# Kernel tuning notes

Measured on AMD Instinct MI355X. Metric: run time of the kernel, lower is better.

The kernel has to match this reference:

```python
import jax, jax.numpy as jnp
import numpy as np
import math

NEG_INF = -1e29
B, L, H = 16, 1024, 512
D = 2 * H          # feature dim of s and q
GELU_C = math.sqrt(2.0 / math.pi)


def gelu(x):
    return 0.5 * x * (1.0 + jnp.tanh(GELU_C * (x + 0.044715 * x ** 3)))


def mask_softmax(W, m1, m2):
    # joint mask: [B, len1, 1] * [B, 1, len2]
    m = (m1[:, :, None] * m2[:, None, :]).astype(W.dtype)
    return jax.nn.softmax(W + (1.0 - m) * NEG_INF, axis=-1)


def heuristic(x, y, w_r, b_r, w_g, b_g):
    inp = jnp.concatenate([x, y, x * y, x - y], axis=-1)  # [B, L, 8H]
    r = gelu(inp @ w_r.T + b_r)                           # [B, L, 2H]
    g = jax.nn.sigmoid(inp @ w_g.T + b_g)
    return g * r + (1.0 - g) * x


def setup_inputs() -> dict:
    key = jax.random.key(0)
    k = jax.random.split(key, 6)
    s = jax.random.normal(k[0], (B, L, D), jnp.float32)
    q = jax.random.normal(k[1], (B, L, D), jnp.float32)
    s_mask = jnp.ones((B, L), jnp.int32)
    q_mask = jnp.ones((B, L), jnp.int32)
    fan_in = 8 * H
    lim = 1.0 / np.sqrt(fan_in)
    w_r = jax.random.uniform(k[2], (2 * H, fan_in), jnp.float32, -lim, lim)
    b_r = jax.random.uniform(k[3], (2 * H,), jnp.float32, -lim, lim)
    w_g = jax.random.uniform(k[4], (2 * H, fan_in), jnp.float32, -lim, lim)
    b_g = jax.random.uniform(k[5], (2 * H,), jnp.float32, -lim, lim)
    return {"s": s, "q": q, "w_r": w_r, "b_r": b_r, "w_g": w_g, "b_g": b_g,
            "s_mask": s_mask, "q_mask": q_mask}


def reference(s, q, w_r, b_r, w_g, b_g, s_mask, q_mask):
    a = jnp.einsum('bsd,btd->bst', s, q)                  # [B, Ls, Lq]
    b = mask_softmax(a, s_mask, q_mask) @ q               # [B, Ls, D]
    c = mask_softmax(a.swapaxes(-1, -2), q_mask, s_mask) @ s  # [B, Lq, D]
    s_tilde = heuristic(s, b, w_r, b_r, w_g, b_g)
    q_tilde = heuristic(q, c, w_r, b_r, w_g, b_g)
    return (s_tilde, q_tilde)
```

## Files before the change

kernel.cpp:

```cpp
#include <hip/hip_runtime.h>
#include <hip/hip_bf16.h>
#include <math.h>

#define DEVI static __device__ __forceinline__

typedef unsigned short u16;
typedef unsigned int u32;
typedef __bf16 bf16_t;
typedef bf16_t bf16x8 __attribute__((ext_vector_type(8)));
typedef float f32x4 __attribute__((ext_vector_type(4)));

static constexpr int Bb = 16;
static constexpr int L  = 1024;
static constexpr int D  = 1024;
static constexpr int KH = 4096;

DEVI u16 f2bf(float f) {
  union { float f; u32 u; } v; v.f = f;
  u32 r = v.u + 0x7FFFu + ((v.u >> 16) & 1u);
  return (u16)(r >> 16);
}

DEVI float bf2f(u16 b) {
  union { u32 u; float f; } v; v.u = ((u32)b) << 16;
  return v.f;
}

DEVI void gload16(const void* g, void* l) {
  __builtin_amdgcn_global_load_lds((const __attribute__((address_space(1))) u32*)g,
                                   (__attribute__((address_space(3))) u32*)l,
                                   16, 0, 0);
}

DEVI int swz(int row, int col) { return col ^ ((row & 7) << 3); }

__global__ void k_cast_bf16(const float* __restrict__ in, u16* __restrict__ out, int n4) {
  int i = blockIdx.x * blockDim.x + threadIdx.x;
  int stride = gridDim.x * blockDim.x;
  for (; i < n4; i += stride) {
    float4 v = ((const float4*)in)[i];
    ushort4 o;
    o.x = f2bf(v.x); o.y = f2bf(v.y); o.z = f2bf(v.z); o.w = f2bf(v.w);
    ((ushort4*)out)[i] = o;
  }
}

__global__ void k_cast_split(const float* __restrict__ in, u16* __restrict__ hi,
                             u16* __restrict__ lo, int n4) {
  int i = blockIdx.x * blockDim.x + threadIdx.x;
  int stride = gridDim.x * blockDim.x;
  for (; i < n4; i += stride) {
    float4 v = ((const float4*)in)[i];
    ushort4 h, l;
    h.x = f2bf(v.x); h.y = f2bf(v.y); h.z = f2bf(v.z); h.w = f2bf(v.w);
    l.x = f2bf(v.x - bf2f(h.x));
    l.y = f2bf(v.y - bf2f(h.y));
    l.z = f2bf(v.z - bf2f(h.z));
    l.w = f2bf(v.w - bf2f(h.w));
    ((ushort4*)hi)[i] = h;
    ((ushort4*)lo)[i] = l;
  }
}

__global__ __launch_bounds__(256)
void k_transpose_bf16(const float* __restrict__ in, u16* __restrict__ out) {
  __shared__ float tile[32][33];
  int b = blockIdx.z;
  int d0 = blockIdx.x * 32;
  int l0 = blockIdx.y * 32;
  const float* ip = in + (size_t)b * L * D;
  u16* op = out + (size_t)b * L * D;
  int tx = threadIdx.x, ty = threadIdx.y;
  #pragma unroll
  for (int j = 0; j < 4; ++j)
    tile[ty + 8 * j][tx] = ip[(size_t)(l0 + ty + 8 * j) * D + d0 + tx];
  __syncthreads();
  #pragma unroll
  for (int j = 0; j < 4; ++j)
    op[(size_t)(d0 + ty + 8 * j) * L + l0 + tx] = f2bf(tile[tx][ty + 8 * j]);
}

template<int OUT_BF16>
__global__ __launch_bounds__(256, 4)
void k_gemm_nt(const u16* __restrict__ A, const u16* __restrict__ Bm, void* __restrict__ Cv,
               int K, int ldc, size_t sA, size_t sB, size_t sC, int tilesN)
{
  __shared__ __align__(16) u16 As[128 * 64];
  __shared__ __align__(16) u16 Bs[128 * 64];
  const int bx = blockIdx.x;
  const int tm = bx / tilesN, tn = bx % tilesN;
  const int b = blockIdx.y;
  const u16* Ap = A + (size_t)b * sA + (size_t)tm * 128 * K;
  const u16* Bp = Bm + (size_t)b * sB + (size_t)tn * 128 * K;
  const int tid = threadIdx.x;
  const int lane = tid & 63, wv = tid >> 6;
  const int wm = wv >> 1, wn = wv & 1;
  const int srow = tid >> 3;
  const int scol = (tid & 7) * 8;
  const int scolswz = swz(srow, scol);
  f32x4 acc[4][4] = {};
  for (int k0 = 0; k0 < K; k0 += 64) {
    #pragma unroll
    for (int i = 0; i < 4; ++i) {
      int row = i * 32 + srow;
      gload16(Ap + (size_t)row * K + k0 + scolswz, &As[row * 64 + scol]);
    }
    #pragma unroll
    for (int i = 0; i < 4; ++i) {
      int row = i * 32 + srow;
      gload16(Bp + (size_t)row * K + k0 + scolswz, &Bs[row * 64 + scol]);
    }
    __syncthreads();
    const int hi8 = (lane >> 4) * 8;
    #pragma unroll
    for (int kk = 0; kk < 64; kk += 32) {
      bf16x8 af[4], bfv[4];
      #pragma unroll
      for (int m = 0; m < 4; ++m) {
        int rr = wm * 64 + m * 16 + (lane & 15);
        af[m] = *(const bf16x8*)&As[rr * 64 + swz(rr, kk + hi8)];
      }
      #pragma unroll
      for (int n = 0; n < 4; ++n) {
        int rr = wn * 64 + n * 16 + (lane & 15);
        bfv[n] = *(const bf16x8*)&Bs[rr * 64 + swz(rr, kk + hi8)];
      }
      #pragma unroll
      for (int m = 0; m < 4; ++m)
        #pragma unroll
        for (int n = 0; n < 4; ++n)
          acc[m][n] = __builtin_amdgcn_mfma_f32_16x16x32_bf16(af[m], bfv[n], acc[m][n], 0, 0, 0);
    }
    __syncthreads();
  }
  const int rb = tm * 128 + wm * 64 + ((lane >> 4) << 2);
  const int cb = tn * 128 + wn * 64 + (lane & 15);
  #pragma unroll
  for (int m = 0; m < 4; ++m)
    #pragma unroll
    for (int n = 0; n < 4; ++n)
      #pragma unroll
      for (int j = 0; j < 4; ++j) {
        int r = rb + m * 16 + j, c = cb + n * 16;
        if (OUT_BF16)
          ((u16*)Cv)[(size_t)b * sC + (size_t)r * ldc + c] = f2bf(acc[m][n][j]);
        else
          ((float*)Cv)[(size_t)b * sC + (size_t)r * ldc + c] = acc[m][n][j];
      }
}

__global__ __launch_bounds__(256, 2)
void k_gemm_nt_split(const u16* __restrict__ Ah, const u16* __restrict__ Al,
                     const u16* __restrict__ Bh, const u16* __restrict__ Bl,
                     float* __restrict__ C, int K, int ldc, size_t sAB, size_t sC, int tilesN)
{
  __shared__ __align__(16) u16 Ahs[128 * 64];
  __shared__ __align__(16) u16 Als[128 * 64];
  __shared__ __align__(16) u16 Bhs[128 * 64];
  __shared__ __align__(16) u16 Bls[128 * 64];
  const int bx = blockIdx.x;
  const int tm = bx / tilesN, tn = bx % tilesN;
  const int b = blockIdx.y;
  const size_t aoff = (size_t)b * sAB + (size_t)tm * 128 * K;
  const size_t boff = (size_t)b * sAB + (size_t)tn * 128 * K;
  const int tid = threadIdx.x;
  const int lane = tid & 63, wv = tid >> 6;
  const int wm = wv >> 1, wn = wv & 1;
  const int srow = tid >> 3;
  const int scol = (tid & 7) * 8;
  const int scolswz = swz(srow, scol);
  f32x4 acc[4][4] = {};
  for (int k0 = 0; k0 < K; k0 += 64) {
    #pragma unroll
    for (int i = 0; i < 4; ++i) {
      int row = i * 32 + srow;
      size_t ga = aoff + (size_t)row * K + k0 + scolswz;
      size_t gb = boff + (size_t)row * K + k0 + scolswz;
      int ls = row * 64 + scol;
      gload16(Ah + ga, &Ahs[ls]);
      gload16(Al + ga, &Als[ls]);
      gload16(Bh + gb, &Bhs[ls]);
      gload16(Bl + gb, &Bls[ls]);
    }
    __syncthreads();
    const int hi8 = (lane >> 4) * 8;
    #pragma unroll
    for (int kk = 0; kk < 64; kk += 32) {
      bf16x8 ah[4], al[4], bh[4], bl[4];
      #pragma unroll
      for (int m = 0; m < 4; ++m) {
        int rr = wm * 64 + m * 16 + (lane & 15);
        int off = rr * 64 + swz(rr, kk + hi8);
        ah[m] = *(const bf16x8*)&Ahs[off];
        al[m] = *(const bf16x8*)&Als[off];
      }
      #pragma unroll
      for (int n = 0; n < 4; ++n) {
        int rr = wn * 64 + n * 16 + (lane & 15);
        int off = rr * 64 + swz(rr, kk + hi8);
        bh[n] = *(const bf16x8*)&Bhs[off];
        bl[n] = *(const bf16x8*)&Bls[off];
      }
      #pragma unroll
      for (int m = 0; m < 4; ++m)
        #pragma unroll
        for (int n = 0; n < 4; ++n) {
          acc[m][n] = __builtin_amdgcn_mfma_f32_16x16x32_bf16(ah[m], bh[n], acc[m][n], 0, 0, 0);
          acc[m][n] = __builtin_amdgcn_mfma_f32_16x16x32_bf16(ah[m], bl[n], acc[m][n], 0, 0, 0);
          acc[m][n] = __builtin_amdgcn_mfma_f32_16x16x32_bf16(al[m], bh[n], acc[m][n], 0, 0, 0);
        }
    }
    __syncthreads();
  }
  const int rb = tm * 128 + wm * 64 + ((lane >> 4) << 2);
  const int cb = tn * 128 + wn * 64 + (lane & 15);
  #pragma unroll
  for (int m = 0; m < 4; ++m)
    #pragma unroll
    for (int n = 0; n < 4; ++n)
      #pragma unroll
      for (int j = 0; j < 4; ++j) {
        int r = rb + m * 16 + j, c = cb + n * 16;
        C[(size_t)b * sC + (size_t)r * ldc + c] = acc[m][n][j];
      }
}

__global__ __launch_bounds__(256)
void k_row_softmax(const float* __restrict__ a, u16* __restrict__ P,
                   const int* __restrict__ m1, const int* __restrict__ m2)
{
  const int row = blockIdx.x, b = blockIdx.y;
  const float* ar = a + ((size_t)b * L + row) * L;
  const int tid = threadIdx.x, lane = tid & 63, wv = tid >> 6;
  __shared__ float redm[4], reds[4];
  float4 v = ((const float4*)ar)[tid];
  int4 mv = ((const int4*)(m2 + (size_t)b * L))[tid];
  const int mr = m1[(size_t)b * L + row];
  float x0 = v.x + (float)(1 - mr * mv.x) * (-1e29f);
  float x1 = v.y + (float)(1 - mr * mv.y) * (-1e29f);
  float x2 = v.z + (float)(1 - mr * mv.z) * (-1e29f);
  float x3 = v.w + (float)(1 - mr * mv.w) * (-1e29f);
  float mx = fmaxf(fmaxf(x0, x1), fmaxf(x2, x3));
  #pragma unroll
  for (int o = 32; o > 0; o >>= 1) mx = fmaxf(mx, __shfl_xor(mx, o));
  if (lane == 0) redm[wv] = mx;
  __syncthreads();
  mx = fmaxf(fmaxf(redm[0], redm[1]), fmaxf(redm[2], redm[3]));
  float e0 = __expf(x0 - mx), e1 = __expf(x1 - mx), e2 = __expf(x2 - mx), e3 = __expf(x3 - mx);
  float s4 = e0 + e1 + e2 + e3;
  #pragma unroll
  for (int o = 32; o > 0; o >>= 1) s4 += __shfl_xor(s4, o);
  if (lane == 0) reds[wv] = s4;
  __syncthreads();
  float inv = 1.0f / (reds[0] + reds[1] + reds[2] + reds[3]);
  ushort4 o;
  o.x = f2bf(e0 * inv); o.y = f2bf(e1 * inv); o.z = f2bf(e2 * inv); o.w = f2bf(e3 * inv);
  ((ushort4*)(P + ((size_t)b * L + row) * L))[tid] = o;
}

__global__ __launch_bounds__(256)
void k_col_softmax(const float* __restrict__ a, u16* __restrict__ P,
                   const int* __restrict__ mrow, const int* __restrict__ mcol)
{
  __shared__ float mred[4][64], lred[4][64];
  __shared__ float Mc[64], Li[64];
  __shared__ u16 T[64][68];
  const int b = blockIdx.y;
  const int c0 = blockIdx.x * 64;
  const int tid = threadIdx.x;
  const int cl = tid & 63;
  const int qr = tid >> 6;
  const int c = c0 + cl;
  const float* ab = a + (size_t)b * L * L;
  const int mc = mcol[(size_t)b * L + c];
  const int* msk = mrow + (size_t)b * L;
  float m = -3.0e38f, l = 0.0f;
  for (int r = qr * 256; r < qr * 256 + 256; ++r) {
    float x = ab[(size_t)r * L + c] + (float)(1 - mc * msk[r]) * (-1e29f);
    float mn = fmaxf(m, x);
    l = l * __expf(m - mn) + __expf(x - mn);
    m = mn;
  }
  mred[qr][cl] = m; lred[qr][cl] = l;
  __syncthreads();
  if (tid < 64) {
    float M = fmaxf(fmaxf(mred[0][tid], mred[1][tid]), fmaxf(mred[2][tid], mred[3][tid]));
    float Lt = lred[0][tid] * __expf(mred[0][tid] - M) + lred[1][tid] * __expf(mred[1][tid] - M)
             + lred[2][tid] * __expf(mred[2][tid] - M) + lred[3][tid] * __expf(mred[3][tid] - M);
    Mc[tid] = M; Li[tid] = 1.0f / Lt;
  }
  __syncthreads();
  const float M = Mc[cl], Linv = Li[cl];
  u16* Pb = P + (size_t)b * L * L;
  const int tl = tid >> 2, sc = (tid & 3) * 16;
  for (int ch = 0; ch < 16; ++ch) {
    #pragma unroll
    for (int rs = 0; rs < 16; ++rs) {
      int r = ch * 64 + qr * 16 + rs;
      float x = ab[(size_t)r * L + c] + (float)(1 - mc * msk[r]) * (-1e29f);
      T[cl][qr * 16 + rs] = f2bf(__expf(x - M) * Linv);
    }
    __syncthreads();
    ushort4* d4 = (ushort4*)(Pb + (size_t)(c0 + tl) * L + ch * 64 + sc);
    #pragma unroll
    for (int jj = 0; jj < 4; ++jj) {
      ushort4 v;
      v.x = T[tl][sc + jj * 4 + 0]; v.y = T[tl][sc + jj * 4 + 1];
      v.z = T[tl][sc + jj * 4 + 2]; v.w = T[tl][sc + jj * 4 + 3];
      d4[jj] = v;
    }
    __syncthreads();
  }
}

__global__ __launch_bounds__(512, 2)
void k_heur2(const u16* __restrict__ Xbf, const u16* __restrict__ Ybf,
             const u16* __restrict__ Wr, const u16* __restrict__ Wg,
             const float* __restrict__ br, const float* __restrict__ bg,
             const float* __restrict__ Xf, float* __restrict__ out)
{
  __shared__ __align__(16) u16 Xs[256 * 64];
  __shared__ __align__(16) u16 Ys[256 * 64];
  __shared__ __align__(16) u16 Ws[2][2][128 * 64];
  const int bx = blockIdx.x;
  const int xcd = bx & 7, li = bx >> 3;
  const int tn = li & 7, tm = xcd * 8 + (li >> 3);
  const size_t rowBase = (size_t)tm * 256;
  const int tid = threadIdx.x, lane = tid & 63;
  const int wv = tid >> 6;
  const int wm = wv >> 1, wn = wv & 1;
  const int srow = tid >> 3;
  const int scol = (tid & 7) * 8;
  const int scolswz = swz(srow, scol);
  f32x4 accR[4][4] = {}, accG[4][4] = {};

  for (int g = 0; g < 16; ++g) {
    const int c0 = g * 64;
    #pragma unroll
    for (int i = 0; i < 4; ++i) {
      int row = i * 64 + srow;
      size_t goff = (rowBase + row) * (size_t)D + c0 + scolswz;
      gload16(Xbf + goff, &Xs[row * 64 + scol]);
      gload16(Ybf + goff, &Ys[row * 64 + scol]);
    }
    #pragma unroll
    for (int i = 0; i < 2; ++i) {
      int row = i * 64 + srow;
      size_t woff = ((size_t)tn * 128 + row) * (size_t)KH + c0 + scolswz;
      gload16(Wr + woff, &Ws[0][0][row * 64 + scol]);
      gload16(Wg + woff, &Ws[0][1][row * 64 + scol]);
    }
    __syncthreads();
    #pragma unroll
    for (int ft = 0; ft < 4; ++ft) {
      const int cur = ft & 1;
      if (ft < 3) {
        #pragma unroll
        for (int i = 0; i < 2; ++i) {
          int row = i * 64 + srow;
          size_t woff = ((size_t)tn * 128 + row) * (size_t)KH + ((ft + 1) * 1024 + c0) + scolswz;
          gload16(Wr + woff, &Ws[cur ^ 1][0][row * 64 + scol]);
          gload16(Wg + woff, &Ws[cur ^ 1][1][row * 64 + scol]);
        }
      }
      const int hi8 = (lane >> 4) * 8;
      #pragma unroll
      for (int kk = 0; kk < 64; kk += 32) {
        bf16x8 af[4];
        #pragma unroll
        for (int m = 0; m < 4; ++m) {
          int rr = wm * 64 + m * 16 + (lane & 15);
          int off = rr * 64 + swz(rr, kk + hi8);
          if (ft == 0) af[m] = *(const bf16x8*)&Xs[off];
          else if (ft == 1) af[m] = *(const bf16x8*)&Ys[off];
          else {
            bf16x8 xv = *(const bf16x8*)&Xs[off];
            bf16x8 yv = *(const bf16x8*)&Ys[off];
            bf16x8 f;
            #pragma unroll
            for (int j = 0; j < 8; ++j) {
              float xf2 = (float)xv[j], yf2 = (float)yv[j];
              f[j] = (bf16_t)((ft == 2) ? xf2 * yf2 : xf2 - yf2);
            }
            af[m] = f;
          }
        }
        #pragma unroll
        for (int n = 0; n < 4; ++n) {
          int rr = wn * 64 + n * 16 + (lane & 15);
          int off = rr * 64 + swz(rr, kk + hi8);
          bf16x8 bR = *(const bf16x8*)&Ws[cur][0][off];
          bf16x8 bG = *(const bf16x8*)&Ws[cur][1][off];
          #pragma unroll
          for (int m = 0; m < 4; ++m) {
            accR[m][n] = __builtin_amdgcn_mfma_f32_16x16x32_bf16(af[m], bR, accR[m][n], 0, 0, 0);
            accG[m][n] = __builtin_amdgcn_mfma_f32_16x16x32_bf16(af[m], bG, accG[m][n], 0, 0, 0);
          }
        }
      }
      __syncthreads();
    }
  }
  const int rb = wm * 64 + ((lane >> 4) << 2);
  const int cb = tn * 128 + wn * 64 + (lane & 15);
  #pragma unroll
  for (int m = 0; m < 4; ++m)
    #pragma unroll
    for (int n = 0; n < 4; ++n)
      #pragma unroll
      for (int j = 0; j < 4; ++j) {
        size_t row = rowBase + rb + m * 16 + j;
        int col = cb + n * 16;
        float r = accR[m][n][j] + br[col];
        float g = accG[m][n][j] + bg[col];
        float t = tanhf(0.79788456080286535588f * (r + 0.044715f * r * r * r));
        float gl = 0.5f * r * (1.0f + t);
        float sg = 1.0f / (1.0f + __expf(-g));
        float xv = Xf[row * (size_t)D + col];
        out[row * (size_t)D + col] = sg * gl + (1.0f - sg) * xv;
      }
}

extern "C" void kernel_launch(void* const* d_in, const int* in_sizes, int n_in,
                              void* d_out, int out_size, void* d_ws, size_t ws_size,
                              hipStream_t stream)
{
  (void)in_sizes; (void)n_in; (void)out_size; (void)ws_size;
  const float* s    = (const float*)d_in[0];
  const float* q    = (const float*)d_in[1];
  const float* w_r  = (const float*)d_in[2];
  const float* b_r  = (const float*)d_in[3];
  const float* w_g  = (const float*)d_in[4];
  const float* b_g  = (const float*)d_in[5];
  const int* s_mask = (const int*)d_in[6];
  const int* q_mask = (const int*)d_in[7];
  float* out = (float*)d_out;

  const size_t SQ = (size_t)Bb * L * D;
  const size_t W  = (size_t)D * KH;
  const size_t S1 = (size_t)L * D;

  char* p = (char*)d_ws;
  u16* s_bf  = (u16*)p; p += SQ * 2;
  u16* q_bf  = (u16*)p; p += SQ * 2;
  u16* buf1  = (u16*)p; p += SQ * 2;
  u16* buf2  = (u16*)p; p += SQ * 2;
  u16* b_bf  = (u16*)p; p += SQ * 2;
  u16* c_bf  = (u16*)p; p += SQ * 2;
  u16* wr_bf = (u16*)p; p += W * 2;
  u16* wg_bf = (u16*)p; p += W * 2;

  float* a  = out;
  u16*   P1 = (u16*)(out + SQ);
  u16*   P2 = (u16*)(out + SQ + SQ / 2);

  dim3 blk(256);
  k_cast_split<<<4096, blk, 0, stream>>>(s, s_bf, buf1, (int)(SQ / 4));
  k_cast_split<<<4096, blk, 0, stream>>>(q, q_bf, buf2, (int)(SQ / 4));
  k_cast_bf16<<<2048, blk, 0, stream>>>(w_r, wr_bf, (int)(W / 4));
  k_cast_bf16<<<2048, blk, 0, stream>>>(w_g, wg_bf, (int)(W / 4));

  dim3 ggrid(64, Bb);
  k_gemm_nt_split<<<ggrid, blk, 0, stream>>>(s_bf, buf1, q_bf, buf2, a, D, L, S1, (size_t)L * L, 8);
  k_row_softmax<<<dim3(L, Bb), blk, 0, stream>>>(a, P1, s_mask, q_mask);
  k_col_softmax<<<dim3(L / 64, Bb), blk, 0, stream>>>(a, P2, s_mask, q_mask);

  dim3 tgrid(D / 32, L / 32, Bb), tblk(32, 8);
  k_transpose_bf16<<<tgrid, tblk, 0, stream>>>(s, buf1);
  k_transpose_bf16<<<tgrid, tblk, 0, stream>>>(q, buf2);

  k_gemm_nt<1><<<ggrid, blk, 0, stream>>>(P1, buf2, b_bf, L, D, (size_t)L * L, S1, S1, 8);
  k_gemm_nt<1><<<ggrid, blk, 0, stream>>>(P2, buf1, c_bf, L, D, (size_t)L * L, S1, S1, 8);

  k_heur2<<<512, dim3(512), 0, stream>>>(s_bf, b_bf, wr_bf, wg_bf, b_r, b_g, s, out);
  k_heur2<<<512, dim3(512), 0, stream>>>(q_bf, c_bf, wr_bf, wg_bf, b_r, b_g, q, out + SQ);
}
```

Measured before the change: 1.060 ms.

## Interleave gate and residual weights and precompute heuristic features for single-GEMM tile

Interleaves the rows of w_r and w_g into one bf16 weight matrix so each output tile computes the r and g columns together with a single accumulator set. A new elementwise kernel precomputes x*y and x-y into buffers, so the GEMM no longer builds those features in its inner loop. The GEMM is restructured to 256x256 tiles with K-step 32, double-buffered LDS, explicit waitcnt and barrier scheduling, and priority boosts around the MFMAs. The epilogue pairs r and g through a lane shuffle, and only even lanes store. In exchange it adds extra global writes and reads for the feature buffers, and half the lanes do redundant epilogue work.

```diff
diff --git a/kernel.cpp b/kernel.cpp
--- a/kernel.cpp
+++ b/kernel.cpp
@@ -59,6 +59,40 @@
     l.w = f2bf(v.w - bf2f(h.w));
     ((ushort4*)hi)[i] = h;
     ((ushort4*)lo)[i] = l;
+  }
+}
+
+__global__ void k_wcat(const float* __restrict__ wr, const float* __restrict__ wg,
+                       u16* __restrict__ wcat, int n4) {
+  int i = blockIdx.x * blockDim.x + threadIdx.x;
+  int stride = gridDim.x * blockDim.x;
+  for (; i < n4; i += stride) {
+    int j = i >> 10;
+    int c4 = i & 1023;
+    const float* src = ((j & 1) ? wg : wr) + (size_t)(j >> 1) * 4096 + c4 * 4;
+    float4 v = *(const float4*)src;
+    ushort4 o;
+    o.x = f2bf(v.x); o.y = f2bf(v.y); o.z = f2bf(v.z); o.w = f2bf(v.w);
+    ((ushort4*)wcat)[i] = o;
+  }
+}
+
+__global__ void k_feat(const u16* __restrict__ x, const u16* __restrict__ y,
+                       u16* __restrict__ xy, u16* __restrict__ xmy, int n8) {
+  int i = blockIdx.x * blockDim.x + threadIdx.x;
+  int stride = gridDim.x * blockDim.x;
+  for (; i < n8; i += stride) {
+    bf16x8 xv = ((const bf16x8*)x)[i];
+    bf16x8 yv = ((const bf16x8*)y)[i];
+    bf16x8 p, d;
+    #pragma unroll
+    for (int j = 0; j < 8; ++j) {
+      float xf = (float)xv[j], yf = (float)yv[j];
+      p[j] = (bf16_t)(xf * yf);
+      d[j] = (bf16_t)(xf - yf);
+    }
+    ((bf16x8*)xy)[i] = p;
+    ((bf16x8*)xmy)[i] = d;
   }
 }
 
@@ -314,111 +348,107 @@
 }
 
 __global__ __launch_bounds__(512, 2)
-void k_heur2(const u16* __restrict__ Xbf, const u16* __restrict__ Ybf,
-             const u16* __restrict__ Wr, const u16* __restrict__ Wg,
-             const float* __restrict__ br, const float* __restrict__ bg,
-             const float* __restrict__ Xf, float* __restrict__ out)
+void k_gemm_heur(const u16* __restrict__ X, const u16* __restrict__ Y,
+                 const u16* __restrict__ XY, const u16* __restrict__ XMY,
+                 const u16* __restrict__ Wc,
+                 const float* __restrict__ br, const float* __restrict__ bg,
+                 const float* __restrict__ Xf, float* __restrict__ out)
 {
-  __shared__ __align__(16) u16 Xs[256 * 64];
-  __shared__ __align__(16) u16 Ys[256 * 64];
-  __shared__ __align__(16) u16 Ws[2][2][128 * 64];
+  __shared__ __align__(16) u16 As[2][256 * 32];
+  __shared__ __align__(16) u16 Bs[2][256 * 32];
   const int bx = blockIdx.x;
   const int xcd = bx & 7, li = bx >> 3;
   const int tn = li & 7, tm = xcd * 8 + (li >> 3);
   const size_t rowBase = (size_t)tm * 256;
-  const int tid = threadIdx.x, lane = tid & 63;
-  const int wv = tid >> 6;
-  const int wm = wv >> 1, wn = wv & 1;
-  const int srow = tid >> 3;
-  const int scol = (tid & 7) * 8;
-  const int scolswz = swz(srow, scol);
-  f32x4 accR[4][4] = {}, accG[4][4] = {};
-
-  for (int g = 0; g < 16; ++g) {
-    const int c0 = g * 64;
-    #pragma unroll
-    for (int i = 0; i < 4; ++i) {
-      int row = i * 64 + srow;
-      size_t goff = (rowBase + row) * (size_t)D + c0 + scolswz;
-      gload16(Xbf + goff, &Xs[row * 64 + scol]);
-      gload16(Ybf + goff, &Ys[row * 64 + scol]);
-    }
-    #pragma unroll
-    for (int i = 0; i < 2; ++i) {
-      int row = i * 64 + srow;
-      size_t woff = ((size_t)tn * 128 + row) * (size_t)KH + c0 + scolswz;
-      gload16(Wr + woff, &Ws[0][0][row * 64 + scol]);
-      gload16(Wg + woff, &Ws[0][1][row * 64 + scol]);
-    }
-    __syncthreads();
-    #pragma unroll
-    for (int ft = 0; ft < 4; ++ft) {
-      const int cur = ft & 1;
-      if (ft < 3) {
-        #pragma unroll
-        for (int i = 0; i < 2; ++i) {
-          int row = i * 64 + srow;
-          size_t woff = ((size_t)tn * 128 + row) * (size_t)KH + ((ft + 1) * 1024 + c0) + scolswz;
-          gload16(Wr + woff, &Ws[cur ^ 1][0][row * 64 + scol]);
-          gload16(Wg + woff, &Ws[cur ^ 1][1][row * 64 + scol]);
-        }
-      }
-      const int hi8 = (lane >> 4) * 8;
-      #pragma unroll
-      for (int kk = 0; kk < 64; kk += 32) {
-        bf16x8 af[4];
-        #pragma unroll
-        for (int m = 0; m < 4; ++m) {
-          int rr = wm * 64 + m * 16 + (lane & 15);
-          int off = rr * 64 + swz(rr, kk + hi8);
-          if (ft == 0) af[m] = *(const bf16x8*)&Xs[off];
-          else if (ft == 1) af[m] = *(const bf16x8*)&Ys[off];
-          else {
-            bf16x8 xv = *(const bf16x8*)&Xs[off];
-            bf16x8 yv = *(const bf16x8*)&Ys[off];
-            bf16x8 f;
-            #pragma unroll
-            for (int j = 0; j < 8; ++j) {
-              float xf2 = (float)xv[j], yf2 = (float)yv[j];
-              f[j] = (bf16_t)((ft == 2) ? xf2 * yf2 : xf2 - yf2);
-            }
-            af[m] = f;
-          }
-        }
-        #pragma unroll
-        for (int n = 0; n < 4; ++n) {
-          int rr = wn * 64 + n * 16 + (lane & 15);
-          int off = rr * 64 + swz(rr, kk + hi8);
-          bf16x8 bR = *(const bf16x8*)&Ws[cur][0][off];
-          bf16x8 bG = *(const bf16x8*)&Ws[cur][1][off];
-          #pragma unroll
-          for (int m = 0; m < 4; ++m) {
-            accR[m][n] = __builtin_amdgcn_mfma_f32_16x16x32_bf16(af[m], bR, accR[m][n], 0, 0, 0);
-            accG[m][n] = __builtin_amdgcn_mfma_f32_16x16x32_bf16(af[m], bG, accG[m][n], 0, 0, 0);
-          }
-        }
-      }
-      __syncthreads();
-    }
-  }
-  const int rb = wm * 64 + ((lane >> 4) << 2);
-  const int cb = tn * 128 + wn * 64 + (lane & 15);
-  #pragma unroll
-  for (int m = 0; m < 4; ++m)
-    #pragma unroll
-    for (int n = 0; n < 4; ++n)
+  const int colBase = tn * 256;
+  const int tid = threadIdx.x, lane = tid & 63, wv = tid >> 6;
+  const int wm = wv >> 2, wn = wv & 3;
+
+  const int sidx0 = (wv * 2 + 0) * 64 + lane;
+  const int sidx1 = (wv * 2 + 1) * 64 + lane;
+  const int arow0 = sidx0 >> 2, arow1 = sidx1 >> 2;
+  const int asl0 = (sidx0 & 3) ^ ((arow0 >> 1) & 3);
+  const int asl1 = (sidx1 & 3) ^ ((arow1 >> 1) & 3);
+  const size_t aoff0 = (rowBase + arow0) * (size_t)D + asl0 * 8;
+  const size_t aoff1 = (rowBase + arow1) * (size_t)D + asl1 * 8;
+  const size_t boff0 = (size_t)(colBase + arow0) * KH + asl0 * 8;
+  const size_t boff1 = (size_t)(colBase + arow1) * KH + asl1 * 8;
+
+  f32x4 acc[8][4] = {};
+
+#define HSTAGE(T, BUF) do {                                                    \
+    int kk0 = (T) * 32;                                                        \
+    const u16* ap = (kk0 < 2048) ? (kk0 < 1024 ? X : Y)                        \
+                                 : (kk0 < 3072 ? XY : XMY);                    \
+    int kc = kk0 & 1023;                                                       \
+    gload16(ap + aoff0 + kc, &As[BUF][sidx0 * 8]);                             \
+    gload16(ap + aoff1 + kc, &As[BUF][sidx1 * 8]);                             \
+    gload16(Wc + boff0 + kk0, &Bs[BUF][sidx0 * 8]);                            \
+    gload16(Wc + boff1 + kk0, &Bs[BUF][sidx1 * 8]);                            \
+  } while (0)
+
+  HSTAGE(0, 0);
+  for (int t = 0; t < 128; ++t) {
+    const int cur = t & 1;
+    asm volatile("" ::: "memory");
+    __builtin_amdgcn_s_barrier();
+    asm volatile("" ::: "memory");
+    if (t + 1 < 128) {
+      HSTAGE(t + 1, cur ^ 1);
+      asm volatile("s_waitcnt vmcnt(4)" ::: "memory");
+    } else {
+      asm volatile("s_waitcnt vmcnt(0)" ::: "memory");
+    }
+    asm volatile("" ::: "memory");
+    __builtin_amdgcn_s_barrier();
+    asm volatile("" ::: "memory");
+
+    bf16x8 af[8], bfv[4];
+    #pragma unroll
+    for (int m = 0; m < 8; ++m) {
+      int rr = wm * 128 + m * 16 + (lane & 15);
+      int sp = (lane >> 4) ^ ((rr >> 1) & 3);
+      af[m] = *(const bf16x8*)&As[cur][rr * 32 + sp * 8];
+    }
+    #pragma unroll
+    for (int n = 0; n < 4; ++n) {
+      int rr = wn * 64 + n * 16 + (lane & 15);
+      int sp = (lane >> 4) ^ ((rr >> 1) & 3);
+      bfv[n] = *(const bf16x8*)&Bs[cur][rr * 32 + sp * 8];
+    }
+    __builtin_amdgcn_s_setprio(1);
+    #pragma unroll
+    for (int m = 0; m < 8; ++m)
+      #pragma unroll
+      for (int n = 0; n < 4; ++n)
+        acc[m][n] = __builtin_amdgcn_mfma_f32_16x16x32_bf16(af[m], bfv[n], acc[m][n], 0, 0, 0);
+    __builtin_amdgcn_s_setprio(0);
+  }
+#undef HSTAGE
+
+  const int odd = lane & 1;
+  #pragma unroll
+  for (int m = 0; m < 8; ++m)
+    #pragma unroll
+    for (int n = 0; n < 4; ++n) {
+      int ncol = colBase + wn * 64 + n * 16 + (lane & 15);
+      int c = ncol >> 1;
       #pragma unroll
       for (int j = 0; j < 4; ++j) {
-        size_t row = rowBase + rb + m * 16 + j;
-        int col = cb + n * 16;
-        float r = accR[m][n][j] + br[col];
-        float g = accG[m][n][j] + bg[col];
-        float t = tanhf(0.79788456080286535588f * (r + 0.044715f * r * r * r));
-        float gl = 0.5f * r * (1.0f + t);
+        size_t row = rowBase + wm * 128 + m * 16 + ((lane >> 4) << 2) + j;
+        float v = acc[m][n][j];
+        float pv = __shfl_xor(v, 1);
+        float r = odd ? pv : v;
+        float g = odd ? v : pv;
+        r += br[c]; g += bg[c];
+        float th = tanhf(0.79788456080286535588f * (r + 0.044715f * r * r * r));
+        float gl = 0.5f * r * (1.0f + th);
         float sg = 1.0f / (1.0f + __expf(-g));
-        float xv = Xf[row * (size_t)D + col];
-        out[row * (size_t)D + col] = sg * gl + (1.0f - sg) * xv;
-      }
+        float xv = Xf[row * (size_t)D + c];
+        float res = sg * gl + (1.0f - sg) * xv;
+        if (!odd) out[row * (size_t)D + c] = res;
+      }
+    }
 }
 
 extern "C" void kernel_launch(void* const* d_in, const int* in_sizes, int n_in,
@@ -447,8 +477,7 @@
   u16* buf2  = (u16*)p; p += SQ * 2;
   u16* b_bf  = (u16*)p; p += SQ * 2;
   u16* c_bf  = (u16*)p; p += SQ * 2;
-  u16* wr_bf = (u16*)p; p += W * 2;
-  u16* wg_bf = (u16*)p; p += W * 2;
+  u16* wcat  = (u16*)p; p += 2 * W * 2;
 
   float* a  = out;
   u16*   P1 = (u16*)(out + SQ);
@@ -457,8 +486,7 @@
   dim3 blk(256);
   k_cast_split<<<4096, blk, 0, stream>>>(s, s_bf, buf1, (int)(SQ / 4));
   k_cast_split<<<4096, blk, 0, stream>>>(q, q_bf, buf2, (int)(SQ / 4));
-  k_cast_bf16<<<2048, blk, 0, stream>>>(w_r, wr_bf, (int)(W / 4));
-  k_cast_bf16<<<2048, blk, 0, stream>>>(w_g, wg_bf, (int)(W / 4));
+  k_wcat<<<4096, blk, 0, stream>>>(w_r, w_g, wcat, (int)(2 * W / 4));
 
   dim3 ggrid(64, Bb);
   k_gemm_nt_split<<<ggrid, blk, 0, stream>>>(s_bf, buf1, q_bf, buf2, a, D, L, S1, (size_t)L * L, 8);
@@ -472,6 +500,9 @@
   k_gemm_nt<1><<<ggrid, blk, 0, stream>>>(P1, buf2, b_bf, L, D, (size_t)L * L, S1, S1, 8);
   k_gemm_nt<1><<<ggrid, blk, 0, stream>>>(P2, buf1, c_bf, L, D, (size_t)L * L, S1, S1, 8);
 
-  k_heur2<<<512, dim3(512), 0, stream>>>(s_bf, b_bf, wr_bf, wg_bf, b_r, b_g, s, out);
-  k_heur2<<<512, dim3(512), 0, stream>>>(q_bf, c_bf, wr_bf, wg_bf, b_r, b_g, q, out + SQ);
-}
+  k_feat<<<2048, blk, 0, stream>>>(s_bf, b_bf, buf1, buf2, (int)(SQ / 8));
+  k_gemm_heur<<<512, dim3(512), 0, stream>>>(s_bf, b_bf, buf1, buf2, wcat, b_r, b_g, s, out);
+
+  k_feat<<<2048, blk, 0, stream>>>(q_bf, c_bf, buf1, buf2, (int)(SQ / 8));
+  k_gemm_heur<<<512, dim3(512), 0, stream>>>(q_bf, c_bf, buf1, buf2, wcat, b_r, b_g, q, out + SQ);
+}
```

Measured after the change: 1.274 ms. 20.2% more time.

## Flatten heuristic GEMM K-loop into a software-pipelined schedule with explicit waitcnts

Applied to the files above, without the earlier changes.

Replaces the nested group/feature loop of the heuristic GEMM with one flat 64-step loop. Weight tiles are prefetched two steps ahead into the double buffer, and the next X/Y tile is loaded after the last feature step, using explicit vmcnt/lgkmcnt waits and raw s_barrier instead of __syncthreads. MFMA bursts are wrapped in s_setprio so compute waves win issue priority. The aim is to overlap global loads with MFMA work and cut barrier stalls; correctness now depends on the hand-counted wait values.

```diff
diff --git a/kernel.cpp b/kernel.cpp
--- a/kernel.cpp
+++ b/kernel.cpp
@@ -334,73 +334,113 @@
   const int scolswz = swz(srow, scol);
   f32x4 accR[4][4] = {}, accG[4][4] = {};
 
-  for (int g = 0; g < 16; ++g) {
-    const int c0 = g * 64;
-    #pragma unroll
-    for (int i = 0; i < 4; ++i) {
-      int row = i * 64 + srow;
-      size_t goff = (rowBase + row) * (size_t)D + c0 + scolswz;
-      gload16(Xbf + goff, &Xs[row * 64 + scol]);
-      gload16(Ybf + goff, &Ys[row * 64 + scol]);
-    }
+  #pragma unroll
+  for (int i = 0; i < 4; ++i) {
+    int row = i * 64 + srow;
+    size_t goff = (rowBase + row) * (size_t)D + scolswz;
+    gload16(Xbf + goff, &Xs[row * 64 + scol]);
+    gload16(Ybf + goff, &Ys[row * 64 + scol]);
+  }
+  #pragma unroll
+  for (int i = 0; i < 2; ++i) {
+    int row = i * 64 + srow;
+    size_t woff = ((size_t)tn * 128 + row) * (size_t)KH + scolswz;
+    gload16(Wr + woff, &Ws[0][0][row * 64 + scol]);
+    gload16(Wg + woff, &Ws[0][1][row * 64 + scol]);
+  }
+  asm volatile("s_waitcnt vmcnt(0)" ::: "memory");
+  __builtin_amdgcn_sched_barrier(0);
+  __builtin_amdgcn_s_barrier();
+  __builtin_amdgcn_sched_barrier(0);
+  {
     #pragma unroll
     for (int i = 0; i < 2; ++i) {
       int row = i * 64 + srow;
-      size_t woff = ((size_t)tn * 128 + row) * (size_t)KH + c0 + scolswz;
-      gload16(Wr + woff, &Ws[0][0][row * 64 + scol]);
-      gload16(Wg + woff, &Ws[0][1][row * 64 + scol]);
-    }
-    __syncthreads();
-    #pragma unroll
-    for (int ft = 0; ft < 4; ++ft) {
-      const int cur = ft & 1;
-      if (ft < 3) {
-        #pragma unroll
-        for (int i = 0; i < 2; ++i) {
-          int row = i * 64 + srow;
-          size_t woff = ((size_t)tn * 128 + row) * (size_t)KH + ((ft + 1) * 1024 + c0) + scolswz;
-          gload16(Wr + woff, &Ws[cur ^ 1][0][row * 64 + scol]);
-          gload16(Wg + woff, &Ws[cur ^ 1][1][row * 64 + scol]);
+      size_t woff = ((size_t)tn * 128 + row) * (size_t)KH + 1024 + scolswz;
+      gload16(Wr + woff, &Ws[1][0][row * 64 + scol]);
+      gload16(Wg + woff, &Ws[1][1][row * 64 + scol]);
+    }
+  }
+
+  for (int t = 0; t < 64; ++t) {
+    const int cur = t & 1;
+    const int ft = t & 3;
+
+    if (t > 0 && ft == 0) {
+      asm volatile("s_waitcnt vmcnt(4)" ::: "memory");
+      __builtin_amdgcn_sched_barrier(0);
+      __builtin_amdgcn_s_barrier();
+      __builtin_amdgcn_sched_barrier(0);
+    }
+
+    const int hi8 = (lane >> 4) * 8;
+    #pragma unroll
+    for (int kk = 0; kk < 64; kk += 32) {
+      bf16x8 af[4];
+      #pragma unroll
+      for (int m = 0; m < 4; ++m) {
+        int rr = wm * 64 + m * 16 + (lane & 15);
+        int off = rr * 64 + swz(rr, kk + hi8);
+        if (ft == 0) af[m] = *(const bf16x8*)&Xs[off];
+        else if (ft == 1) af[m] = *(const bf16x8*)&Ys[off];
+        else {
+          bf16x8 xv = *(const bf16x8*)&Xs[off];
+          bf16x8 yv = *(const bf16x8*)&Ys[off];
+          bf16x8 f;
+          #pragma unroll
+          for (int j = 0; j < 8; ++j) {
+            float xf2 = (float)xv[j], yf2 = (float)yv[j];
+            f[j] = (bf16_t)((ft == 2) ? xf2 * yf2 : xf2 - yf2);
+          }
+          af[m] = f;
         }
       }
-      const int hi8 = (lane >> 4) * 8;
-      #pragma unroll
-      for (int kk = 0; kk < 64; kk += 32) {
-        bf16x8 af[4];
+      #pragma unroll
+      for (int n = 0; n < 4; ++n) {
+        int rr = wn * 64 + n * 16 + (lane & 15);
+        int off = rr * 64 + swz(rr, kk + hi8);
+        bf16x8 bR = *(const bf16x8*)&Ws[cur][0][off];
+        bf16x8 bG = *(const bf16x8*)&Ws[cur][1][off];
+        __builtin_amdgcn_s_setprio(1);
         #pragma unroll
         for (int m = 0; m < 4; ++m) {
-          int rr = wm * 64 + m * 16 + (lane & 15);
-          int off = rr * 64 + swz(rr, kk + hi8);
-          if (ft == 0) af[m] = *(const bf16x8*)&Xs[off];
-          else if (ft == 1) af[m] = *(const bf16x8*)&Ys[off];
-          else {
-            bf16x8 xv = *(const bf16x8*)&Xs[off];
-            bf16x8 yv = *(const bf16x8*)&Ys[off];
-            bf16x8 f;
-            #pragma unroll
-            for (int j = 0; j < 8; ++j) {
-              float xf2 = (float)xv[j], yf2 = (float)yv[j];
-              f[j] = (bf16_t)((ft == 2) ? xf2 * yf2 : xf2 - yf2);
-            }
-            af[m] = f;
-          }
+          accR[m][n] = __builtin_amdgcn_mfma_f32_16x16x32_bf16(af[m], bR, accR[m][n], 0, 0, 0);
+          accG[m][n] = __builtin_amdgcn_mfma_f32_16x16x32_bf16(af[m], bG, accG[m][n], 0, 0, 0);
         }
-        #pragma unroll
-        for (int n = 0; n < 4; ++n) {
-          int rr = wn * 64 + n * 16 + (lane & 15);
-          int off = rr * 64 + swz(rr, kk + hi8);
-          bf16x8 bR = *(const bf16x8*)&Ws[cur][0][off];
-          bf16x8 bG = *(const bf16x8*)&Ws[cur][1][off];
-          #pragma unroll
-          for (int m = 0; m < 4; ++m) {
-            accR[m][n] = __builtin_amdgcn_mfma_f32_16x16x32_bf16(af[m], bR, accR[m][n], 0, 0, 0);
-            accG[m][n] = __builtin_amdgcn_mfma_f32_16x16x32_bf16(af[m], bG, accG[m][n], 0, 0, 0);
-          }
-        }
-      }
-      __syncthreads();
-    }
-  }
+        __builtin_amdgcn_s_setprio(0);
+      }
+    }
+
+    asm volatile("s_waitcnt lgkmcnt(0)" ::: "memory");
+    __builtin_amdgcn_sched_barrier(0);
+    asm volatile("s_waitcnt vmcnt(0)" ::: "memory");
+    __builtin_amdgcn_sched_barrier(0);
+    __builtin_amdgcn_s_barrier();
+    __builtin_amdgcn_sched_barrier(0);
+
+    if (ft == 3 && t < 60) {
+      int g1 = (t >> 2) + 1;
+      #pragma unroll
+      for (int i = 0; i < 4; ++i) {
+        int row = i * 64 + srow;
+        size_t goff = (rowBase + row) * (size_t)D + g1 * 64 + scolswz;
+        gload16(Xbf + goff, &Xs[row * 64 + scol]);
+        gload16(Ybf + goff, &Ys[row * 64 + scol]);
+      }
+    }
+    if (t < 62) {
+      int t2 = t + 2;
+      int kcol = (t2 & 3) * 1024 + (t2 >> 2) * 64;
+      #pragma unroll
+      for (int i = 0; i < 2; ++i) {
+        int row = i * 64 + srow;
+        size_t woff = ((size_t)tn * 128 + row) * (size_t)KH + kcol + scolswz;
+        gload16(Wr + woff, &Ws[cur][0][row * 64 + scol]);
+        gload16(Wg + woff, &Ws[cur][1][row * 64 + scol]);
+      }
+    }
+  }
+
   const int rb = wm * 64 + ((lane >> 4) << 2);
   const int cb = tn * 128 + wn * 64 + (lane & 15);
   #pragma unroll
@@ -413,8 +453,8 @@
         int col = cb + n * 16;
         float r = accR[m][n][j] + br[col];
         float g = accG[m][n][j] + bg[col];
-        float t = tanhf(0.79788456080286535588f * (r + 0.044715f * r * r * r));
-        float gl = 0.5f * r * (1.0f + t);
+        float th = tanhf(0.79788456080286535588f * (r + 0.044715f * r * r * r));
+        float gl = 0.5f * r * (1.0f + th);
         float sg = 1.0f / (1.0f + __expf(-g));
         float xv = Xf[row * (size_t)D + col];
         out[row * (size_t)D + col] = sg * gl + (1.0f - sg) * xv;
```

New measurement: 1.233 ms. +16.3%, slower.

## Precompute x*y and x-y features and pipeline heuristic GEMM over uniform K tiles

Applied to the files above, without the earlier changes.

Adds a separate elementwise kernel that writes the x*y and x-y bf16 feature blocks to workspace buffers. The heuristic GEMM then streams one A tile per K step from four source arrays and double-buffers both the A and weight tiles in shared memory across all 64 K steps. This removes the per-fragment conversion arithmetic from the MFMA inner loop and the per-group full barrier stall. In exchange it adds extra global traffic: the feature buffers are written and then re-read, and X and Y are now reloaded per K step instead of being reused across four weight slices.

```diff
diff --git a/kernel.cpp b/kernel.cpp
--- a/kernel.cpp
+++ b/kernel.cpp
@@ -59,6 +59,25 @@
     l.w = f2bf(v.w - bf2f(h.w));
     ((ushort4*)hi)[i] = h;
     ((ushort4*)lo)[i] = l;
+  }
+}
+
+__global__ void k_feat(const u16* __restrict__ x, const u16* __restrict__ y,
+                       u16* __restrict__ xy, u16* __restrict__ xmy, int n8) {
+  int i = blockIdx.x * blockDim.x + threadIdx.x;
+  int stride = gridDim.x * blockDim.x;
+  for (; i < n8; i += stride) {
+    bf16x8 xv = ((const bf16x8*)x)[i];
+    bf16x8 yv = ((const bf16x8*)y)[i];
+    bf16x8 p, d;
+    #pragma unroll
+    for (int j = 0; j < 8; ++j) {
+      float xf = (float)xv[j], yf = (float)yv[j];
+      p[j] = (bf16_t)(xf * yf);
+      d[j] = (bf16_t)(xf - yf);
+    }
+    ((bf16x8*)xy)[i] = p;
+    ((bf16x8*)xmy)[i] = d;
   }
 }
 
@@ -314,14 +333,15 @@
 }
 
 __global__ __launch_bounds__(512, 2)
-void k_heur2(const u16* __restrict__ Xbf, const u16* __restrict__ Ybf,
+void k_heur3(const u16* __restrict__ X, const u16* __restrict__ Y,
+             const u16* __restrict__ XY, const u16* __restrict__ XMY,
              const u16* __restrict__ Wr, const u16* __restrict__ Wg,
              const float* __restrict__ br, const float* __restrict__ bg,
              const float* __restrict__ Xf, float* __restrict__ out)
 {
-  __shared__ __align__(16) u16 Xs[256 * 64];
-  __shared__ __align__(16) u16 Ys[256 * 64];
-  __shared__ __align__(16) u16 Ws[2][2][128 * 64];
+  __shared__ __align__(16) u16 As[2][256 * 64];
+  __shared__ __align__(16) u16 Wrs[2][128 * 64];
+  __shared__ __align__(16) u16 Wgs[2][128 * 64];
   const int bx = blockIdx.x;
   const int xcd = bx & 7, li = bx >> 3;
   const int tn = li & 7, tm = xcd * 8 + (li >> 3);
@@ -334,73 +354,57 @@
   const int scolswz = swz(srow, scol);
   f32x4 accR[4][4] = {}, accG[4][4] = {};
 
-  for (int g = 0; g < 16; ++g) {
-    const int c0 = g * 64;
+  auto stage = [&](int t, int buf) {
+    const int fa = t >> 4;
+    const u16* ap = (fa == 0) ? X : (fa == 1) ? Y : (fa == 2) ? XY : XMY;
+    const int kcol = (t & 15) * 64;
     #pragma unroll
     for (int i = 0; i < 4; ++i) {
       int row = i * 64 + srow;
-      size_t goff = (rowBase + row) * (size_t)D + c0 + scolswz;
-      gload16(Xbf + goff, &Xs[row * 64 + scol]);
-      gload16(Ybf + goff, &Ys[row * 64 + scol]);
-    }
+      gload16(ap + (rowBase + row) * (size_t)D + kcol + scolswz, &As[buf][row * 64 + scol]);
+    }
+    const size_t wcol = (size_t)t * 64;
     #pragma unroll
     for (int i = 0; i < 2; ++i) {
       int row = i * 64 + srow;
-      size_t woff = ((size_t)tn * 128 + row) * (size_t)KH + c0 + scolswz;
-      gload16(Wr + woff, &Ws[0][0][row * 64 + scol]);
-      gload16(Wg + woff, &Ws[0][1][row * 64 + scol]);
-    }
-    __syncthreads();
-    #pragma unroll
-    for (int ft = 0; ft < 4; ++ft) {
-      const int cur = ft & 1;
-      if (ft < 3) {
-        #pragma unroll
-        for (int i = 0; i < 2; ++i) {
-          int row = i * 64 + srow;
-          size_t woff = ((size_t)tn * 128 + row) * (size_t)KH + ((ft + 1) * 1024 + c0) + scolswz;
-          gload16(Wr + woff, &Ws[cur ^ 1][0][row * 64 + scol]);
-          gload16(Wg + woff, &Ws[cur ^ 1][1][row * 64 + scol]);
-        }
-      }
-      const int hi8 = (lane >> 4) * 8;
-      #pragma unroll
-      for (int kk = 0; kk < 64; kk += 32) {
-        bf16x8 af[4];
+      size_t woff = ((size_t)tn * 128 + row) * (size_t)KH + wcol + scolswz;
+      gload16(Wr + woff, &Wrs[buf][row * 64 + scol]);
+      gload16(Wg + woff, &Wgs[buf][row * 64 + scol]);
+    }
+  };
+
+  stage(0, 0);
+  __syncthreads();
+
+  for (int t = 0; t < 64; ++t) {
+    const int cur = t & 1;
+    if (t < 63) stage(t + 1, cur ^ 1);
+
+    const int hi8 = (lane >> 4) * 8;
+    #pragma unroll
+    for (int kk = 0; kk < 64; kk += 32) {
+      bf16x8 af[4];
+      #pragma unroll
+      for (int m = 0; m < 4; ++m) {
+        int rr = wm * 64 + m * 16 + (lane & 15);
+        af[m] = *(const bf16x8*)&As[cur][rr * 64 + swz(rr, kk + hi8)];
+      }
+      #pragma unroll
+      for (int n = 0; n < 4; ++n) {
+        int rr = wn * 64 + n * 16 + (lane & 15);
+        int off = rr * 64 + swz(rr, kk + hi8);
+        bf16x8 bR = *(const bf16x8*)&Wrs[cur][off];
+        bf16x8 bG = *(const bf16x8*)&Wgs[cur][off];
         #pragma unroll
         for (int m = 0; m < 4; ++m) {
-          int rr = wm * 64 + m * 16 + (lane & 15);
-          int off = rr * 64 + swz(rr, kk + hi8);
-          if (ft == 0) af[m] = *(const bf16x8*)&Xs[off];
-          else if (ft == 1) af[m] = *(const bf16x8*)&Ys[off];
-          else {
-            bf16x8 xv = *(const bf16x8*)&Xs[off];
-            bf16x8 yv = *(const bf16x8*)&Ys[off];
-            bf16x8 f;
-            #pragma unroll
-            for (int j = 0; j < 8; ++j) {
-              float xf2 = (float)xv[j], yf2 = (float)yv[j];
-              f[j] = (bf16_t)((ft == 2) ? xf2 * yf2 : xf2 - yf2);
-            }
-            af[m] = f;
-          }
+          accR[m][n] = __builtin_amdgcn_mfma_f32_16x16x32_bf16(af[m], bR, accR[m][n], 0, 0, 0);
+          accG[m][n] = __builtin_amdgcn_mfma_f32_16x16x32_bf16(af[m], bG, accG[m][n], 0, 0, 0);
         }
-        #pragma unroll
-        for (int n = 0; n < 4; ++n) {
-          int rr = wn * 64 + n * 16 + (lane & 15);
-          int off = rr * 64 + swz(rr, kk + hi8);
-          bf16x8 bR = *(const bf16x8*)&Ws[cur][0][off];
-          bf16x8 bG = *(const bf16x8*)&Ws[cur][1][off];
-          #pragma unroll
-          for (int m = 0; m < 4; ++m) {
-            accR[m][n] = __builtin_amdgcn_mfma_f32_16x16x32_bf16(af[m], bR, accR[m][n], 0, 0, 0);
-            accG[m][n] = __builtin_amdgcn_mfma_f32_16x16x32_bf16(af[m], bG, accG[m][n], 0, 0, 0);
-          }
-        }
-      }
-      __syncthreads();
-    }
-  }
+      }
+    }
+    __syncthreads();
+  }
+
   const int rb = wm * 64 + ((lane >> 4) << 2);
   const int cb = tn * 128 + wn * 64 + (lane & 15);
   #pragma unroll
@@ -413,8 +417,8 @@
         int col = cb + n * 16;
         float r = accR[m][n][j] + br[col];
         float g = accG[m][n][j] + bg[col];
-        float t = tanhf(0.79788456080286535588f * (r + 0.044715f * r * r * r));
-        float gl = 0.5f * r * (1.0f + t);
+        float th = tanhf(0.79788456080286535588f * (r + 0.044715f * r * r * r));
+        float gl = 0.5f * r * (1.0f + th);
         float sg = 1.0f / (1.0f + __expf(-g));
         float xv = Xf[row * (size_t)D + col];
         out[row * (size_t)D + col] = sg * gl + (1.0f - sg) * xv;
@@ -472,6 +476,9 @@
   k_gemm_nt<1><<<ggrid, blk, 0, stream>>>(P1, buf2, b_bf, L, D, (size_t)L * L, S1, S1, 8);
   k_gemm_nt<1><<<ggrid, blk, 0, stream>>>(P2, buf1, c_bf, L, D, (size_t)L * L, S1, S1, 8);
 
-  k_heur2<<<512, dim3(512), 0, stream>>>(s_bf, b_bf, wr_bf, wg_bf, b_r, b_g, s, out);
-  k_heur2<<<512, dim3(512), 0, stream>>>(q_bf, c_bf, wr_bf, wg_bf, b_r, b_g, q, out + SQ);
-}
+  k_feat<<<2048, blk, 0, stream>>>(s_bf, b_bf, buf1, buf2, (int)(SQ / 8));
+  k_heur3<<<512, dim3(512), 0, stream>>>(s_bf, b_bf, buf1, buf2, wr_bf, wg_bf, b_r, b_g, s, out);
+
+  k_feat<<<2048, blk, 0, stream>>>(q_bf, c_bf, buf1, buf2, (int)(SQ / 8));
+  k_heur3<<<512, dim3(512), 0, stream>>>(q_bf, c_bf, buf1, buf2, wr_bf, wg_bf, b_r, b_g, q, out + SQ);
+}
```

New measurement: 1.042 ms. No clear change (-1.7%).
